# Performance work log

Hardware: AMD Instinct MI355X
Metric: run time of the kernel (lower is better)

## Reference

```python
import jax, jax.numpy as jnp
import numpy as np


def setup_inputs() -> dict:
    key = jax.random.key(0)
    N, H, CH, T = 4, 8, 64, 2048
    qkv = jax.random.normal(key, (N, 3 * H * CH, T), dtype=jnp.float32)
    return {"qkv": qkv, "n_heads": H}


def reference(qkv, n_heads):
    bs, width, length = qkv.shape
    ch = width // (3 * n_heads)
    q, k, v = jnp.split(qkv, 3, axis=1)  # each [bs, H*ch, T]
    q = q.reshape(bs * n_heads, ch, length)
    k = k.reshape(bs * n_heads, ch, length)
    v = v.reshape(bs * n_heads, ch, length)
    scale = 1.0 / jnp.sqrt(jnp.sqrt(jnp.asarray(ch, dtype=qkv.dtype)))
    # [bs*H, T, T] score matrix (non-flash, materialized as in the original)
    weight = jnp.einsum('bct,bcs->bts', q * scale, k * scale)
    weight = jax.nn.softmax(weight.astype(jnp.float32), axis=-1).astype(qkv.dtype)
    a = jnp.einsum('bts,bcs->bct', weight, v)  # [bs*H, ch, T]
    return a.reshape(bs, n_heads * ch, length)
```

## Files before the change

kernel.cpp:

```cpp
#include <hip/hip_runtime.h>


typedef __bf16 bf8v __attribute__((ext_vector_type(8)));
typedef __bf16 bf4 __attribute__((ext_vector_type(4)));
typedef short s4 __attribute__((ext_vector_type(4)));
typedef float f4 __attribute__((ext_vector_type(4)));
typedef int i4 __attribute__((ext_vector_type(4)));

#define SEQ 2048
#define DD 64
#define NHEADS 32
#define QBLK 128
#define SBLK 64
#define NTILES (SEQ / SBLK)
#define TILEK (SBLK * DD)
#define NTHR 256

#define KSC 0.35355339059327373f
#define QSC (0.35355339059327373f * 1.4426950408889634f)

#if __has_builtin(__builtin_amdgcn_exp2f)
#define EXP2(x) __builtin_amdgcn_exp2f(x)
#else
#define EXP2(x) exp2f(x)
#endif

__device__ __forceinline__ void gload16(i4& dst, const __bf16* p) {
    asm volatile("global_load_dwordx4 %0, %1, off" : "=&v"(dst) : "v"(p));
}

#define VMWAIT0() do { asm volatile("s_waitcnt vmcnt(0)" ::: "memory"); \
                       __builtin_amdgcn_sched_barrier(0); } while (0)
#define SBAR() __builtin_amdgcn_sched_barrier(0)

#if __has_builtin(__builtin_amdgcn_mfma_f32_16x16x16bf16_1k)
__device__ __forceinline__ f4 mfma16(bf4 a, bf4 b, f4 c) {
    union U { bf4 v; s4 s; };
    U ua; ua.v = a;
    U ub; ub.v = b;
    return __builtin_amdgcn_mfma_f32_16x16x16bf16_1k(ua.s, ub.s, c, 0, 0, 0);
}
#else
__device__ __forceinline__ f4 mfma16(bf4 a, bf4 b, f4 c) {
    asm("v_mfma_f32_16x16x16_bf16 %0, %1, %2, %0" : "+v"(c) : "v"(a), "v"(b));
    return c;
}
#endif

__global__ void prep_kernel(const float* __restrict__ qkv,
                            __bf16* __restrict__ KT, __bf16* __restrict__ Vb) {
    const int bx = blockIdx.x, tid = threadIdx.x;
    if (bx < 256) {
        const int head = bx >> 3, sblk = bx & 7;
        const int b = head >> 3, h = head & 7;
        const float* kp = qkv + (size_t)(b * 1536 + 512 + h * 64) * SEQ;
        __bf16* dst = KT + (size_t)head * SEQ * DD;
        const int s = sblk * 256 + tid;
#pragma unroll
        for (int c0 = 0; c0 < DD; c0 += 8) {
            bf8v v;
#pragma unroll
            for (int j = 0; j < 8; ++j)
                v[j] = (__bf16)(kp[(size_t)(c0 + j) * SEQ + s] * KSC);
            *(bf8v*)(dst + (size_t)s * DD + c0) = v;
        }
    } else {
        const int job = bx - 256;
        const int head = job >> 4, part = job & 15;
        const int b = head >> 3, h = head & 7;
        const float* vp = qkv + (size_t)(b * 1536 + 1024 + h * 64) * SEQ;
        __bf16* dst = Vb + (size_t)head * DD * SEQ;
#pragma unroll
        for (int i = 0; i < 4; ++i) {
            const int e = part * 8192 + (i * 256 + tid) * 8;
            const float4* f = (const float4*)(vp + e);
            float4 a = f[0], c = f[1];
            bf8v o;
            o[0] = (__bf16)a.x; o[1] = (__bf16)a.y; o[2] = (__bf16)a.z; o[3] = (__bf16)a.w;
            o[4] = (__bf16)c.x; o[5] = (__bf16)c.y; o[6] = (__bf16)c.z; o[7] = (__bf16)c.w;
            *(bf8v*)(dst + e) = o;
        }
    }
}

__device__ __forceinline__ bf8v ldswz(const __bf16* base, int r, int c16) {
    return *(const bf8v*)(base + r * DD + (((c16) ^ (r & 7)) << 3));
}
__device__ __forceinline__ bf4 ldswz4(const __bf16* base, int r, int sloc) {
    const int c16 = sloc >> 3, off = sloc & 7;
    return *(const bf4*)(base + r * DD + (((c16) ^ (r & 7)) << 3) + off);
}

__global__ __launch_bounds__(NTHR, 2) void attn_kernel(
    const float* __restrict__ qkv, const __bf16* __restrict__ KT,
    const __bf16* __restrict__ Vb, float* __restrict__ out)
{
    __shared__ __bf16 KL[2][TILEK];
    __shared__ __bf16 VL[2][TILEK];

    const int tid = threadIdx.x;
    const int wid = tid >> 6;
    const int lane = tid & 63;
    const int g = lane >> 4;
    const int l15 = lane & 15;

    const int bid = blockIdx.x;
    const int bx = (bid & 7) * 64 + (bid >> 3);
    const int head = bx >> 4;
    const int t0 = (bx & 15) * QBLK;
    const int b = head >> 3, h = head & 7;

    const float* qp = qkv + (size_t)(b * 1536 + h * 64) * SEQ;
    const __bf16* kt = KT + (size_t)head * SEQ * DD;
    const __bf16* vb = Vb + (size_t)head * DD * SEQ;
    float* op = out + (size_t)head * DD * SEQ;

    const int sp  = tid & 7;
    const int sr  = tid >> 3;
    const int scs = sp ^ (sr & 7);
    const __bf16* kg0 = kt + sr * DD + (scs << 3);
    const __bf16* kg1 = kt + (sr + 32) * DD + (scs << 3);
    const __bf16* vg0 = vb + (size_t)sr * SEQ + (scs << 3);
    const __bf16* vg1 = vb + (size_t)(sr + 32) * SEQ + (scs << 3);
    const int l0 = sr * DD + (sp << 3);
    const int l1 = (sr + 32) * DD + (sp << 3);

    i4 rk0, rk1, rv0, rv1;

    SBAR();
    gload16(rk0, kg0);
    gload16(rk1, kg1);
    gload16(rv0, vg0);
    gload16(rv1, vg1);
    SBAR();

    bf8v qf[2][2];
    {
        const int tq = t0 + wid * 32 + l15;
#pragma unroll
        for (int ts = 0; ts < 2; ++ts)
#pragma unroll
            for (int ks = 0; ks < 2; ++ks) {
                bf8v q;
#pragma unroll
                for (int j = 0; j < 8; ++j)
                    q[j] = (__bf16)(qp[(size_t)(ks * 32 + g * 8 + j) * SEQ + tq + ts * 16] * QSC);
                qf[ts][ks] = q;
            }
    }

    f4 Oacc[4][2];
#pragma unroll
    for (int ms = 0; ms < 4; ++ms) {
        Oacc[ms][0] = (f4){0.f, 0.f, 0.f, 0.f};
        Oacc[ms][1] = (f4){0.f, 0.f, 0.f, 0.f};
    }
    float lper[2] = {0.f, 0.f};

    VMWAIT0();
    *(i4*)&KL[0][l0] = rk0;  *(i4*)&KL[0][l1] = rk1;
    *(i4*)&VL[0][l0] = rv0;  *(i4*)&VL[0][l1] = rv1;
    __syncthreads();

    for (int it = 0; it < NTILES; ++it) {
        const int cb = it & 1;
        const __bf16* kcu = KL[cb];
        const __bf16* vcu = VL[cb];
        const bool more = (it + 1 < NTILES);

        if (more) {
            const int nx = it + 1;
            SBAR();
            gload16(rk0, kg0 + nx * TILEK);
            gload16(rk1, kg1 + nx * TILEK);
            gload16(rv0, vg0 + nx * SBLK);
            gload16(rv1, vg1 + nx * SBLK);
            SBAR();
        }

        f4 S[4][2];
#pragma unroll
        for (int ss = 0; ss < 4; ++ss) {
            S[ss][0] = (f4){0.f, 0.f, 0.f, 0.f};
            S[ss][1] = (f4){0.f, 0.f, 0.f, 0.f};
        }
        __builtin_amdgcn_s_setprio(1);
#pragma unroll
        for (int ks = 0; ks < 2; ++ks)
#pragma unroll
            for (int ss = 0; ss < 4; ++ss) {
                bf8v a = ldswz(kcu, ss * 16 + l15, ks * 4 + g);
                S[ss][0] = __builtin_amdgcn_mfma_f32_16x16x32_bf16(a, qf[0][ks], S[ss][0], 0, 0, 0);
                S[ss][1] = __builtin_amdgcn_mfma_f32_16x16x32_bf16(a, qf[1][ks], S[ss][1], 0, 0, 0);
            }
        __builtin_amdgcn_s_setprio(0);

        bf4 vf[4][4];
#pragma unroll
        for (int ms = 0; ms < 4; ++ms)
#pragma unroll
            for (int ss = 0; ss < 4; ++ss)
                vf[ms][ss] = ldswz4(vcu, ms * 16 + l15, ss * 16 + g * 4);

        bf4 pb[2][4];
#pragma unroll
        for (int ts = 0; ts < 2; ++ts) {
            float tsum = 0.f;
#pragma unroll
            for (int ss = 0; ss < 4; ++ss) {
                bf4 q;
#pragma unroll
                for (int r = 0; r < 4; ++r) {
                    float e = EXP2(S[ss][ts][r]);
                    tsum += e;
                    q[r] = (__bf16)e;
                }
                pb[ts][ss] = q;
            }
            lper[ts] += tsum;
        }

        if (more) {
            VMWAIT0();
            __bf16* kn = (__bf16*)KL[cb ^ 1];
            __bf16* vn = (__bf16*)VL[cb ^ 1];
            *(i4*)&kn[l0] = rk0;  *(i4*)&kn[l1] = rk1;
            *(i4*)&vn[l0] = rv0;  *(i4*)&vn[l1] = rv1;
            __syncthreads();
        }

        __builtin_amdgcn_s_setprio(1);
#pragma unroll
        for (int ss = 0; ss < 4; ++ss)
#pragma unroll
            for (int ms = 0; ms < 4; ++ms) {
                Oacc[ms][0] = mfma16(vf[ms][ss], pb[0][ss], Oacc[ms][0]);
                Oacc[ms][1] = mfma16(vf[ms][ss], pb[1][ss], Oacc[ms][1]);
            }
        __builtin_amdgcn_s_setprio(0);
    }

    asm volatile("s_nop 7\n\ts_nop 7" :::);

#pragma unroll
    for (int ts = 0; ts < 2; ++ts) {
        float l = lper[ts];
        l += __shfl_xor(l, 16);
        l += __shfl_xor(l, 32);
        const float rl = 1.0f / l;
        const int t = t0 + wid * 32 + ts * 16 + l15;
#pragma unroll
        for (int ms = 0; ms < 4; ++ms)
#pragma unroll
            for (int r = 0; r < 4; ++r)
                op[(size_t)(ms * 16 + g * 4 + r) * SEQ + t] = Oacc[ms][ts][r] * rl;
    }
}

extern "C" void kernel_launch(void* const* d_in, const int* in_sizes, int n_in,
                              void* d_out, int out_size, void* d_ws, size_t ws_size,
                              hipStream_t stream) {
    const float* qkv = (const float*)d_in[0];
    float* out = (float*)d_out;
    __bf16* KT = (__bf16*)d_ws;
    __bf16* Vb = KT + (size_t)NHEADS * SEQ * DD;
    prep_kernel<<<dim3(256 + 512), dim3(NTHR), 0, stream>>>(qkv, KT, Vb);
    attn_kernel<<<dim3(NHEADS * (SEQ / QBLK)), dim3(NTHR), 0, stream>>>(qkv, KT, Vb, out);
}
```

Baseline: 71.05 us.

## Switch attention MFMAs to 32x32x16 tiles with permlane32 swap for P layout

Replaces the 16x16x32 QK and 16x16x16 PV matrix instructions with 32x32x16 bf16 MFMAs, so each wave computes 32 query columns with a single pair of accumulators. The exponentiated scores are repacked with v_permlane32_swap so the S accumulator layout can feed the PV MFMA B operand directly, and V fragments become 8-wide LDS loads. The aim is fewer MFMA issues, fewer and wider LDS reads, and lower per-instruction overhead. It relies on the permlane32 swap producing the right operand layout and adds a small nop for hazard spacing.

Measured after the change: 64.76 us. 1.1x faster.

```diff
diff --git a/kernel.cpp b/kernel.cpp
--- a/kernel.cpp
+++ b/kernel.cpp
@@ -2,9 +2,7 @@
 
 
 typedef __bf16 bf8v __attribute__((ext_vector_type(8)));
-typedef __bf16 bf4 __attribute__((ext_vector_type(4)));
-typedef short s4 __attribute__((ext_vector_type(4)));
-typedef float f4 __attribute__((ext_vector_type(4)));
+typedef float f16v __attribute__((ext_vector_type(16)));
 typedef int i4 __attribute__((ext_vector_type(4)));
 
 #define SEQ 2048
@@ -33,17 +31,16 @@
                        __builtin_amdgcn_sched_barrier(0); } while (0)
 #define SBAR() __builtin_amdgcn_sched_barrier(0)
 
-#if __has_builtin(__builtin_amdgcn_mfma_f32_16x16x16bf16_1k)
-__device__ __forceinline__ f4 mfma16(bf4 a, bf4 b, f4 c) {
-    union U { bf4 v; s4 s; };
-    U ua; ua.v = a;
-    U ub; ub.v = b;
-    return __builtin_amdgcn_mfma_f32_16x16x16bf16_1k(ua.s, ub.s, c, 0, 0, 0);
+#if __has_builtin(__builtin_amdgcn_permlane32_swap)
+typedef int i2v __attribute__((ext_vector_type(2)));
+__device__ __forceinline__ void plswap(unsigned& a, unsigned& b) {
+    i2v r = __builtin_amdgcn_permlane32_swap((int)a, (int)b, false, false);
+    a = (unsigned)r.x;
+    b = (unsigned)r.y;
 }
 #else
-__device__ __forceinline__ f4 mfma16(bf4 a, bf4 b, f4 c) {
-    asm("v_mfma_f32_16x16x16_bf16 %0, %1, %2, %0" : "+v"(c) : "v"(a), "v"(b));
-    return c;
+__device__ __forceinline__ void plswap(unsigned& a, unsigned& b) {
+    asm volatile("v_permlane32_swap_b32 %0, %1" : "+v"(a), "+v"(b));
 }
 #endif
 
@@ -86,10 +83,6 @@
 __device__ __forceinline__ bf8v ldswz(const __bf16* base, int r, int c16) {
     return *(const bf8v*)(base + r * DD + (((c16) ^ (r & 7)) << 3));
 }
-__device__ __forceinline__ bf4 ldswz4(const __bf16* base, int r, int sloc) {
-    const int c16 = sloc >> 3, off = sloc & 7;
-    return *(const bf4*)(base + r * DD + (((c16) ^ (r & 7)) << 3) + off);
-}
 
 __global__ __launch_bounds__(NTHR, 2) void attn_kernel(
     const float* __restrict__ qkv, const __bf16* __restrict__ KT,
@@ -101,8 +94,8 @@
     const int tid = threadIdx.x;
     const int wid = tid >> 6;
     const int lane = tid & 63;
-    const int g = lane >> 4;
-    const int l15 = lane & 15;
+    const int hi = lane >> 5;
+    const int l31 = lane & 31;
 
     const int bid = blockIdx.x;
     const int bx = (bid & 7) * 64 + (bid >> 3);
@@ -134,28 +127,21 @@
     gload16(rv1, vg1);
     SBAR();
 
-    bf8v qf[2][2];
-    {
-        const int tq = t0 + wid * 32 + l15;
-#pragma unroll
-        for (int ts = 0; ts < 2; ++ts)
-#pragma unroll
-            for (int ks = 0; ks < 2; ++ks) {
-                bf8v q;
-#pragma unroll
-                for (int j = 0; j < 8; ++j)
-                    q[j] = (__bf16)(qp[(size_t)(ks * 32 + g * 8 + j) * SEQ + tq + ts * 16] * QSC);
-                qf[ts][ks] = q;
-            }
+    const int tq = t0 + wid * 32 + l31;
+    bf8v qf[4];
+#pragma unroll
+    for (int kb = 0; kb < 4; ++kb) {
+        bf8v q;
+#pragma unroll
+        for (int j = 0; j < 8; ++j)
+            q[j] = (__bf16)(qp[(size_t)(kb * 16 + hi * 8 + j) * SEQ + tq] * QSC);
+        qf[kb] = q;
     }
 
-    f4 Oacc[4][2];
-#pragma unroll
-    for (int ms = 0; ms < 4; ++ms) {
-        Oacc[ms][0] = (f4){0.f, 0.f, 0.f, 0.f};
-        Oacc[ms][1] = (f4){0.f, 0.f, 0.f, 0.f};
-    }
-    float lper[2] = {0.f, 0.f};
+    f16v Oacc[2];
+    Oacc[0] = (f16v)0.0f;
+    Oacc[1] = (f16v)0.0f;
+    float lp[4] = {0.f, 0.f, 0.f, 0.f};
 
     VMWAIT0();
     *(i4*)&KL[0][l0] = rk0;  *(i4*)&KL[0][l1] = rk1;
@@ -178,47 +164,55 @@
             SBAR();
         }
 
-        f4 S[4][2];
-#pragma unroll
-        for (int ss = 0; ss < 4; ++ss) {
-            S[ss][0] = (f4){0.f, 0.f, 0.f, 0.f};
-            S[ss][1] = (f4){0.f, 0.f, 0.f, 0.f};
-        }
+        bf8v ka[2][4];
+#pragma unroll
+        for (int sb = 0; sb < 2; ++sb)
+#pragma unroll
+            for (int kb = 0; kb < 4; ++kb)
+                ka[sb][kb] = ldswz(kcu, sb * 32 + l31, 2 * kb + hi);
+
+        f16v S[2];
+        S[0] = (f16v)0.0f;
+        S[1] = (f16v)0.0f;
         __builtin_amdgcn_s_setprio(1);
 #pragma unroll
-        for (int ks = 0; ks < 2; ++ks)
-#pragma unroll
-            for (int ss = 0; ss < 4; ++ss) {
-                bf8v a = ldswz(kcu, ss * 16 + l15, ks * 4 + g);
-                S[ss][0] = __builtin_amdgcn_mfma_f32_16x16x32_bf16(a, qf[0][ks], S[ss][0], 0, 0, 0);
-                S[ss][1] = __builtin_amdgcn_mfma_f32_16x16x32_bf16(a, qf[1][ks], S[ss][1], 0, 0, 0);
+        for (int kb = 0; kb < 4; ++kb) {
+            S[0] = __builtin_amdgcn_mfma_f32_32x32x16_bf16(ka[0][kb], qf[kb], S[0], 0, 0, 0);
+            S[1] = __builtin_amdgcn_mfma_f32_32x32x16_bf16(ka[1][kb], qf[kb], S[1], 0, 0, 0);
+        }
+        __builtin_amdgcn_s_setprio(0);
+
+        bf8v vf[2][4];
+#pragma unroll
+        for (int vcb = 0; vcb < 2; ++vcb)
+#pragma unroll
+            for (int kb = 0; kb < 4; ++kb)
+                vf[vcb][kb] = ldswz(vcu, vcb * 32 + l31, 2 * kb + hi);
+
+        unsigned pd[2][4][2];
+#pragma unroll
+        for (int sb = 0; sb < 2; ++sb)
+#pragma unroll
+            for (int q = 0; q < 4; ++q) {
+                float e0 = EXP2(S[sb][4 * q + 0]);
+                float e1 = EXP2(S[sb][4 * q + 1]);
+                float e2 = EXP2(S[sb][4 * q + 2]);
+                float e3 = EXP2(S[sb][4 * q + 3]);
+                lp[q] += (e0 + e1) + (e2 + e3);
+                union { __bf16 h[2]; unsigned u; } p0, p1;
+                p0.h[0] = (__bf16)e0; p0.h[1] = (__bf16)e1;
+                p1.h[0] = (__bf16)e2; p1.h[1] = (__bf16)e3;
+                pd[sb][q][0] = p0.u;
+                pd[sb][q][1] = p1.u;
             }
-        __builtin_amdgcn_s_setprio(0);
-
-        bf4 vf[4][4];
-#pragma unroll
-        for (int ms = 0; ms < 4; ++ms)
-#pragma unroll
-            for (int ss = 0; ss < 4; ++ss)
-                vf[ms][ss] = ldswz4(vcu, ms * 16 + l15, ss * 16 + g * 4);
-
-        bf4 pb[2][4];
-#pragma unroll
-        for (int ts = 0; ts < 2; ++ts) {
-            float tsum = 0.f;
-#pragma unroll
-            for (int ss = 0; ss < 4; ++ss) {
-                bf4 q;
-#pragma unroll
-                for (int r = 0; r < 4; ++r) {
-                    float e = EXP2(S[ss][ts][r]);
-                    tsum += e;
-                    q[r] = (__bf16)e;
-                }
-                pb[ts][ss] = q;
+
+#pragma unroll
+        for (int sb = 0; sb < 2; ++sb)
+#pragma unroll
+            for (int m = 0; m < 2; ++m) {
+                plswap(pd[sb][2 * m][0], pd[sb][2 * m + 1][0]);
+                plswap(pd[sb][2 * m][1], pd[sb][2 * m + 1][1]);
             }
-            lper[ts] += tsum;
-        }
 
         if (more) {
             VMWAIT0();
@@ -229,32 +223,35 @@
             __syncthreads();
         }
 
+        asm volatile("s_nop 2" :::);
+
         __builtin_amdgcn_s_setprio(1);
 #pragma unroll
-        for (int ss = 0; ss < 4; ++ss)
-#pragma unroll
-            for (int ms = 0; ms < 4; ++ms) {
-                Oacc[ms][0] = mfma16(vf[ms][ss], pb[0][ss], Oacc[ms][0]);
-                Oacc[ms][1] = mfma16(vf[ms][ss], pb[1][ss], Oacc[ms][1]);
+        for (int sb = 0; sb < 2; ++sb)
+#pragma unroll
+            for (int m = 0; m < 2; ++m) {
+                const int kb = 2 * sb + m;
+                union { unsigned u[4]; bf8v b; } f;
+                f.u[0] = pd[sb][2 * m][0];
+                f.u[1] = pd[sb][2 * m][1];
+                f.u[2] = pd[sb][2 * m + 1][0];
+                f.u[3] = pd[sb][2 * m + 1][1];
+                Oacc[0] = __builtin_amdgcn_mfma_f32_32x32x16_bf16(vf[0][kb], f.b, Oacc[0], 0, 0, 0);
+                Oacc[1] = __builtin_amdgcn_mfma_f32_32x32x16_bf16(vf[1][kb], f.b, Oacc[1], 0, 0, 0);
             }
         __builtin_amdgcn_s_setprio(0);
     }
 
-    asm volatile("s_nop 7\n\ts_nop 7" :::);
-
-#pragma unroll
-    for (int ts = 0; ts < 2; ++ts) {
-        float l = lper[ts];
-        l += __shfl_xor(l, 16);
-        l += __shfl_xor(l, 32);
-        const float rl = 1.0f / l;
-        const int t = t0 + wid * 32 + ts * 16 + l15;
-#pragma unroll
-        for (int ms = 0; ms < 4; ++ms)
-#pragma unroll
-            for (int r = 0; r < 4; ++r)
-                op[(size_t)(ms * 16 + g * 4 + r) * SEQ + t] = Oacc[ms][ts][r] * rl;
-    }
+    float l = (lp[0] + lp[1]) + (lp[2] + lp[3]);
+    l += __shfl_xor(l, 32);
+    const float rl = 1.0f / l;
+#pragma unroll
+    for (int cbk = 0; cbk < 2; ++cbk)
+#pragma unroll
+        for (int r = 0; r < 16; ++r) {
+            const int row = cbk * 32 + (r & 3) + 8 * (r >> 2) + 4 * hi;
+            op[(size_t)row * SEQ + tq] = Oacc[cbk][r] * rl;
+        }
 }
 
 extern "C" void kernel_launch(void* const* d_in, const int* in_sizes, int n_in,
```
